# Optimization experiments

Measured on AMD Instinct MI355X. Metric: run time of the kernel, lower is better.

Reference implementation:

```python
import jax, jax.numpy as jnp
import numpy as np

D_MODEL = 1024
N_HEADS = 16
HEAD_DIM = D_MODEL // N_HEADS
ROPE_BASE = 10000.0


def setup_inputs() -> dict:
    key = jax.random.key(0)
    ks = jax.random.split(key, 9)
    s = 0.02
    inp = {
        "x": jax.random.normal(ks[0], (2, 2048, D_MODEL), dtype=jnp.float32),
        "Wq": jax.random.normal(ks[1], (D_MODEL, D_MODEL), dtype=jnp.float32) * s,
        "bq": jnp.zeros((D_MODEL,), dtype=jnp.float32),
        "Wk": jax.random.normal(ks[2], (D_MODEL, D_MODEL), dtype=jnp.float32) * s,
        "bk": jnp.zeros((D_MODEL,), dtype=jnp.float32),
        "Wv": jax.random.normal(ks[3], (D_MODEL, D_MODEL), dtype=jnp.float32) * s,
        "bv": jnp.zeros((D_MODEL,), dtype=jnp.float32),
        "Wo": jax.random.normal(ks[4], (D_MODEL, D_MODEL), dtype=jnp.float32) * s,
        "bo": jnp.zeros((D_MODEL,), dtype=jnp.float32),
    }
    return inp


def _rope_cos_sin(T, head_dim, dtype):
    inv_freq = 1.0 / (ROPE_BASE ** (jnp.arange(0, head_dim, 2, dtype=jnp.float32) / head_dim))
    pos = jnp.arange(T, dtype=jnp.float32)
    freqs = jnp.outer(pos, inv_freq)              # [T, head_dim/2]
    emb = jnp.concatenate([freqs, freqs], axis=-1)  # [T, head_dim]
    return jnp.cos(emb).astype(dtype), jnp.sin(emb).astype(dtype)


def _rotate_half(x):
    x1, x2 = jnp.split(x, 2, axis=-1)
    return jnp.concatenate([-x2, x1], axis=-1)


def reference(x, Wq, bq, Wk, bk, Wv, bv, Wo, bo):
    B, T, _ = x.shape
    H, Dh = N_HEADS, HEAD_DIM
    # projections (torch Linear: x @ W.T + b)
    q = (x @ Wq.T + bq).reshape(B, T, H, Dh).transpose(0, 2, 1, 3)  # [B,H,T,Dh]
    k = (x @ Wk.T + bk).reshape(B, T, H, Dh).transpose(0, 2, 1, 3)
    v = (x @ Wv.T + bv).reshape(B, T, H, Dh).transpose(0, 2, 1, 3)
    cos, sin = _rope_cos_sin(T, Dh, x.dtype)  # [T, Dh]
    cos = cos[None, None]
    sin = sin[None, None]
    q = q * cos + _rotate_half(q) * sin
    k = k * cos + _rotate_half(k) * sin
    scale = 1.0 / jnp.sqrt(jnp.asarray(Dh, dtype=x.dtype))
    attn = jnp.einsum("bhqd,bhkd->bhqk", q, k) * scale
    attn = jax.nn.softmax(attn, axis=-1)
    out = jnp.einsum("bhqk,bhkd->bhqd", attn, v)  # [B,H,T,Dh]
    out = out.transpose(0, 2, 1, 3).reshape(B, T, H * Dh)
    return out @ Wo.T + bo
```

## Files before the change

kernel.cpp:

```cpp
#include <hip/hip_runtime.h>
#include <hip/hip_bf16.h>
#include <cstdint>

#define D_MODEL 1024
#define NHEADS 16
#define HDIM 64
#define SEQ 2048
#define NBATCH 2
#define BT (NBATCH * SEQ)

typedef short bf16x8 __attribute__((ext_vector_type(8)));
typedef float f32x4 __attribute__((ext_vector_type(4)));
typedef unsigned short u16;
typedef unsigned int u32;

__device__ inline u16 f2bf(float f) {
    union { float f; u32 u; } x;
    x.f = f;
    u32 r = (x.u + 0x7fffu + ((x.u >> 16) & 1u)) >> 16;
    return (u16)r;
}

__device__ inline u32 pack2bf(float a, float b) {
    union { __hip_bfloat162 h; u32 u; } c;
    c.h = __float22bfloat162_rn(float2{a, b});
    return c.u;
}

__device__ inline float bf2f(u16 v) {
    union { u32 u; float f; } x;
    x.u = ((u32)v) << 16;
    return x.f;
}

__device__ inline void async_copy16(const u16* g, u16* l) {
    __builtin_amdgcn_global_load_lds((const __attribute__((address_space(1))) void*)g,
                                     (__attribute__((address_space(3))) void*)l, 16, 0, 0);
}

__device__ inline void permswap32(u32& a, u32& b) {
    asm("v_permlane32_swap_b32 %0, %1" : "+v"(a), "+v"(b));
}
__device__ inline void permswap16(u32& a, u32& b) {
    asm("v_permlane16_swap_b32 %0, %1" : "+v"(a), "+v"(b));
}

#define X4 (BT * D_MODEL / 4)
#define W4 (D_MODEL * D_MODEL / 4)
#define ROPE_N (SEQ * 32)

__global__ void prep_kernel(const float* __restrict__ x,
                            const float* __restrict__ wq, const float* __restrict__ wk,
                            const float* __restrict__ wv, const float* __restrict__ wo,
                            u16* __restrict__ xb,
                            u16* __restrict__ dq, u16* __restrict__ dk,
                            u16* __restrict__ dv, u16* __restrict__ dow,
                            float2* __restrict__ csT) {
    int idx = blockIdx.x * blockDim.x + threadIdx.x;
    if (idx < X4) {
        float4 v = ((const float4*)x)[idx];
        ushort4 o;
        o.x = f2bf(v.x); o.y = f2bf(v.y); o.z = f2bf(v.z); o.w = f2bf(v.w);
        ((ushort4*)xb)[idx] = o;
    } else if (idx < X4 + 4 * W4) {
        int j = idx - X4;
        int w = j >> 18, i = j & (W4 - 1);
        const float* s = (w == 0) ? wq : (w == 1) ? wk : (w == 2) ? wv : wo;
        u16* d = (w == 0) ? dq : (w == 1) ? dk : (w == 2) ? dv : dow;
        float4 v = ((const float4*)s)[i];
        ushort4 o;
        o.x = f2bf(v.x); o.y = f2bf(v.y); o.z = f2bf(v.z); o.w = f2bf(v.w);
        ((ushort4*)d)[i] = o;
    } else {
        int j = idx - (X4 + 4 * W4);
        if (j < ROPE_N) {
            int t = j >> 5, dm = j & 31;
            float invf = exp2f(-(float)dm * (13.287712379549449f / 32.0f));
            float ang = (float)t * invf;
            float s, c;
            sincosf(ang, &s, &c);
            csT[t * 32 + dm] = float2{c, s};
        }
    }
}

#define QSCALE 0.1803368801111204f
#define VPAD 132

__global__ __launch_bounds__(256) void gemm_qkv_kernel(
    const u16* __restrict__ xb,
    const u16* __restrict__ wqb, const u16* __restrict__ wkb, const u16* __restrict__ wvb,
    const float* __restrict__ bq, const float* __restrict__ bk, const float* __restrict__ bv,
    const float2* __restrict__ csT,
    u16* __restrict__ Qb, u16* __restrict__ Kb, u16* __restrict__ VTb) {
    __shared__ __align__(16) u16 smem[128 * VPAD];

    const int z = blockIdx.z;
    const u16* Bw = (z == 0) ? wqb : (z == 1) ? wkb : wvb;
    const float* bias = (z == 0) ? bq : (z == 1) ? bk : bv;

    const int tid = threadIdx.x;
    const int lane = tid & 63, wave = tid >> 6;
    const int waveM = wave >> 1, waveN = wave & 1;
    const int quad = lane >> 4, l16 = lane & 15;

    f32x4 acc[4][4];
#pragma unroll
    for (int mt = 0; mt < 4; ++mt)
#pragma unroll
        for (int nt = 0; nt < 4; ++nt)
            acc[mt][nt] = (f32x4){0.f, 0.f, 0.f, 0.f};

    const int srow = tid >> 2;
    const int scol = (tid & 3) << 3;
    const u16* Ag0 = xb + (size_t)(blockIdx.x * 128 + srow) * D_MODEL + scol;
    const u16* Ag1 = Ag0 + (size_t)64 * D_MODEL;
    const u16* Bg0 = Bw + (size_t)(blockIdx.y * 128 + srow) * D_MODEL + scol;
    const u16* Bg1 = Bg0 + (size_t)64 * D_MODEL;
    const int sidx = srow * 32 + scol;
    u16* As = smem;
    u16* Bs = smem + 8192;

    uint4 a0 = *(const uint4*)&Ag0[0];
    uint4 a1 = *(const uint4*)&Ag1[0];
    uint4 b0 = *(const uint4*)&Bg0[0];
    uint4 b1 = *(const uint4*)&Bg1[0];
    *(uint4*)&As[sidx] = a0;
    *(uint4*)&As[sidx + 2048] = a1;
    *(uint4*)&Bs[sidx] = b0;
    *(uint4*)&Bs[sidx + 2048] = b1;
    a0 = *(const uint4*)&Ag0[32];
    a1 = *(const uint4*)&Ag1[32];
    b0 = *(const uint4*)&Bg0[32];
    b1 = *(const uint4*)&Bg1[32];
    __syncthreads();

#pragma unroll 2
    for (int it = 0; it < 32; ++it) {
        const int cur = it & 1;
        if (it < 31) {
            u16* Ad = As + (cur ^ 1) * 4096;
            u16* Bd = Bs + (cur ^ 1) * 4096;
            *(uint4*)&Ad[sidx] = a0;
            *(uint4*)&Ad[sidx + 2048] = a1;
            *(uint4*)&Bd[sidx] = b0;
            *(uint4*)&Bd[sidx + 2048] = b1;
        }
        if (it < 30) {
            const int k = (it + 2) * 32;
            a0 = *(const uint4*)&Ag0[k];
            a1 = *(const uint4*)&Ag1[k];
            b0 = *(const uint4*)&Bg0[k];
            b1 = *(const uint4*)&Bg1[k];
        }
        const u16* Ac = As + cur * 4096;
        const u16* Bc = Bs + cur * 4096;
        bf16x8 af[4], bfr[4];
#pragma unroll
        for (int mt = 0; mt < 4; ++mt)
            af[mt] = *(const bf16x8*)&Ac[(waveM * 64 + mt * 16 + l16) * 32 + quad * 8];
#pragma unroll
        for (int nt = 0; nt < 4; ++nt)
            bfr[nt] = *(const bf16x8*)&Bc[(waveN * 64 + nt * 16 + l16) * 32 + quad * 8];
#pragma unroll
        for (int mt = 0; mt < 4; ++mt)
#pragma unroll
            for (int nt = 0; nt < 4; ++nt)
                acc[mt][nt] = __builtin_amdgcn_mfma_f32_16x16x32_bf16(af[mt], bfr[nt], acc[mt][nt], 0, 0, 0);
        __syncthreads();
    }

    const int gm0 = blockIdx.x * 128 + waveM * 64 + quad * 4;
    const int gn0 = blockIdx.y * 128 + waveN * 64 + l16;

    float bvv[4];
#pragma unroll
    for (int nt = 0; nt < 4; ++nt) bvv[nt] = bias[gn0 + nt * 16];
#pragma unroll
    for (int mt = 0; mt < 4; ++mt)
#pragma unroll
        for (int nt = 0; nt < 4; ++nt)
#pragma unroll
            for (int r = 0; r < 4; ++r) acc[mt][nt][r] += bvv[nt];

    if (z < 2) {
        u16* dst = (z == 0) ? Qb : Kb;
        const float post = (z == 0) ? QSCALE : 1.0f;
        const int h = 2 * blockIdx.y + waveN;
#pragma unroll
        for (int mt = 0; mt < 4; ++mt) {
#pragma unroll
            for (int r = 0; r < 4; ++r) {
                int gm = gm0 + mt * 16 + r;
                int t = gm & (SEQ - 1), b = gm >> 11;
                float2 cs0 = csT[t * 32 + l16];
                float2 cs1 = csT[t * 32 + 16 + l16];
                float a0f = acc[mt][0][r], a1f = acc[mt][1][r];
                float a2f = acc[mt][2][r], a3f = acc[mt][3][r];
                size_t base = ((size_t)(b * NHEADS + h) * SEQ + t) * HDIM;
                dst[base + l16]      = f2bf((a0f * cs0.x - a2f * cs0.y) * post);
                dst[base + l16 + 16] = f2bf((a1f * cs1.x - a3f * cs1.y) * post);
                dst[base + l16 + 32] = f2bf((a2f * cs0.x + a0f * cs0.y) * post);
                dst[base + l16 + 48] = f2bf((a3f * cs1.x + a1f * cs1.y) * post);
            }
        }
    } else {
        __syncthreads();
#pragma unroll
        for (int mt = 0; mt < 4; ++mt) {
            int t_local = waveM * 64 + mt * 16 + quad * 4;
#pragma unroll
            for (int nt = 0; nt < 4; ++nt) {
                int n_local = waveN * 64 + nt * 16 + l16;
                uint2 w;
                w.x = pack2bf(acc[mt][nt][0], acc[mt][nt][1]);
                w.y = pack2bf(acc[mt][nt][2], acc[mt][nt][3]);
                *(uint2*)&smem[n_local * VPAD + t_local] = w;
            }
        }
        __syncthreads();
        const int row = tid >> 1;
        const int hc = (tid & 1) * 64;
        const int n_g = blockIdx.y * 128 + row;
        const int h = n_g >> 6, d = n_g & 63;
        const int b = (blockIdx.x * 128) >> 11;
        const int t0 = ((blockIdx.x * 128) & (SEQ - 1)) + hc;
        u16* dst = &VTb[((size_t)(b * NHEADS + h) * HDIM + d) * SEQ + t0];
        const u16* src = &smem[row * VPAD + hc];
#pragma unroll
        for (int j = 0; j < 8; ++j)
            *(int4*)&dst[j * 8] = *(const int4*)&src[j * 8];
    }
}

#define LPAD 72

__global__ __launch_bounds__(256, 2) void flash_kernel(
    const u16* __restrict__ Qb, const u16* __restrict__ Kb, const u16* __restrict__ VTb,
    u16* __restrict__ Po0, u16* __restrict__ Po1, float* __restrict__ Ls) {
    __shared__ __align__(16) u16 Ks[2][64 * LPAD];
    __shared__ __align__(16) u16 VTs[2][64 * LPAD];

    const int tid = threadIdx.x;
    const int wave = tid >> 6, lane = tid & 63;
    const int quad = lane >> 4, l16 = lane & 15;
    const int bh = blockIdx.y;
    const int hf = blockIdx.z;
    const u16* Qh = Qb + (size_t)bh * SEQ * HDIM;
    const u16* Kh = Kb + ((size_t)bh * SEQ + hf * (SEQ / 2)) * HDIM;
    const u16* Vh = VTb + (size_t)bh * HDIM * SEQ + hf * (SEQ / 2);
    const int qblk = blockIdx.x * 256 + wave * 64;

    bf16x8 aq[4][2];
#pragma unroll
    for (int nt2 = 0; nt2 < 4; ++nt2)
#pragma unroll
        for (int ks = 0; ks < 2; ++ks)
            aq[nt2][ks] = *(const bf16x8*)&Qh[(qblk + nt2 * 16 + l16) * HDIM + ks * 32 + quad * 8];

    f32x4 o[4][4];
    float lsum[4] = {0.f, 0.f, 0.f, 0.f};
#pragma unroll
    for (int mt2 = 0; mt2 < 4; ++mt2)
#pragma unroll
        for (int nt = 0; nt < 4; ++nt) o[mt2][nt] = (f32x4){0.f, 0.f, 0.f, 0.f};

    const int lr = tid >> 2;
    const int lc = (tid & 3) * 16;
    const u16* Kg = Kh + (size_t)lr * HDIM + lc;
    const u16* Vg = Vh + (size_t)lr * SEQ + lc;
    const int sidx = lr * LPAD + lc;

    uint4 ka, kc, va, vc;
    ka = *(const uint4*)&Kg[0];
    kc = *(const uint4*)&Kg[8];
    va = *(const uint4*)&Vg[0];
    vc = *(const uint4*)&Vg[8];
    *(uint4*)&Ks[0][sidx] = ka;
    *(uint4*)&Ks[0][sidx + 8] = kc;
    *(uint4*)&VTs[0][sidx] = va;
    *(uint4*)&VTs[0][sidx + 8] = vc;
    ka = *(const uint4*)&Kg[(size_t)64 * HDIM];
    kc = *(const uint4*)&Kg[(size_t)64 * HDIM + 8];
    va = *(const uint4*)&Vg[64];
    vc = *(const uint4*)&Vg[64 + 8];
    __syncthreads();

#pragma unroll 2
    for (int it = 0; it < 16; ++it) {
        const int cur = it & 1;
        if (it < 15) {
            *(uint4*)&Ks[cur ^ 1][sidx] = ka;
            *(uint4*)&Ks[cur ^ 1][sidx + 8] = kc;
            *(uint4*)&VTs[cur ^ 1][sidx] = va;
            *(uint4*)&VTs[cur ^ 1][sidx + 8] = vc;
        }
        if (it < 14) {
            ka = *(const uint4*)&Kg[(size_t)(it + 2) * 64 * HDIM];
            kc = *(const uint4*)&Kg[(size_t)(it + 2) * 64 * HDIM + 8];
            va = *(const uint4*)&Vg[(it + 2) * 64];
            vc = *(const uint4*)&Vg[(it + 2) * 64 + 8];
        }
        const u16* Ksc = Ks[cur];
        const u16* Vsc = VTs[cur];

        f32x4 sacc[4][4];
#pragma unroll
        for (int mt = 0; mt < 4; ++mt)
#pragma unroll
            for (int nt2 = 0; nt2 < 4; ++nt2) sacc[mt][nt2] = (f32x4){0.f, 0.f, 0.f, 0.f};
#pragma unroll
        for (int ks = 0; ks < 2; ++ks) {
            bf16x8 kf[4];
#pragma unroll
            for (int mt = 0; mt < 4; ++mt)
                kf[mt] = *(const bf16x8*)&Ksc[(mt * 16 + l16) * LPAD + ks * 32 + quad * 8];
#pragma unroll
            for (int mt = 0; mt < 4; ++mt)
#pragma unroll
                for (int nt2 = 0; nt2 < 4; ++nt2)
                    sacc[mt][nt2] = __builtin_amdgcn_mfma_f32_16x16x32_bf16(kf[mt], aq[nt2][ks], sacc[mt][nt2], 0, 0, 0);
        }

        u32 pq[4][2][4];
#pragma unroll
        for (int nt2 = 0; nt2 < 4; ++nt2) {
            u32 w[4][2];
#pragma unroll
            for (int mt = 0; mt < 4; ++mt) {
                float p0 = __builtin_amdgcn_exp2f(sacc[mt][nt2][0]);
                float p1 = __builtin_amdgcn_exp2f(sacc[mt][nt2][1]);
                float p2 = __builtin_amdgcn_exp2f(sacc[mt][nt2][2]);
                float p3 = __builtin_amdgcn_exp2f(sacc[mt][nt2][3]);
                lsum[nt2] += (p0 + p1) + (p2 + p3);
                w[mt][0] = pack2bf(p0, p1);
                w[mt][1] = pack2bf(p2, p3);
            }
#pragma unroll
            for (int ks = 0; ks < 2; ++ks)
#pragma unroll
                for (int h = 0; h < 2; ++h) {
                    u32 a = w[2 * ks][h], b = w[2 * ks + 1][h];
                    permswap32(a, b);
                    permswap16(a, b);
                    pq[nt2][ks][h] = a;
                    pq[nt2][ks][2 + h] = b;
                }
        }

#pragma unroll
        for (int ks = 0; ks < 2; ++ks) {
            bf16x8 vf[4];
#pragma unroll
            for (int nt = 0; nt < 4; ++nt)
                vf[nt] = *(const bf16x8*)&Vsc[(nt * 16 + l16) * LPAD + ks * 32 + quad * 8];
#pragma unroll
            for (int mt2 = 0; mt2 < 4; ++mt2) {
                union { u32 u[4]; bf16x8 v; } pf;
                pf.u[0] = pq[mt2][ks][0];
                pf.u[1] = pq[mt2][ks][1];
                pf.u[2] = pq[mt2][ks][2];
                pf.u[3] = pq[mt2][ks][3];
#pragma unroll
                for (int nt = 0; nt < 4; ++nt)
                    o[mt2][nt] = __builtin_amdgcn_mfma_f32_16x16x32_bf16(pf.v, vf[nt], o[mt2][nt], 0, 0, 0);
            }
        }
        __syncthreads();
    }

#pragma unroll
    for (int nt2 = 0; nt2 < 4; ++nt2) {
        lsum[nt2] += __shfl_xor(lsum[nt2], 16, 64);
        lsum[nt2] += __shfl_xor(lsum[nt2], 32, 64);
    }

    const int b = bh >> 4, h = bh & 15;
    u16* dst = hf ? Po1 : Po0;
#pragma unroll
    for (int mt2 = 0; mt2 < 4; ++mt2) {
#pragma unroll
        for (int nt = 0; nt < 4; ++nt) {
            int d = nt * 16 + l16;
#pragma unroll
            for (int r = 0; r < 4; ++r) {
                int q = qblk + mt2 * 16 + quad * 4 + r;
                dst[((size_t)(b * SEQ + q)) * D_MODEL + h * HDIM + d] = f2bf(o[mt2][nt][r]);
            }
        }
    }
    if (quad == 0) {
#pragma unroll
        for (int nt2 = 0; nt2 < 4; ++nt2) {
            int q = qblk + nt2 * 16 + l16;
            Ls[hf * (32 * SEQ) + bh * SEQ + q] = lsum[nt2];
        }
    }
}

__global__ __launch_bounds__(256) void gemm_out_kernel(
    const u16* __restrict__ Po0, const u16* __restrict__ Po1, const float* __restrict__ Ls,
    const u16* __restrict__ wob, const float* __restrict__ bo, float* __restrict__ dout) {
    __shared__ __align__(16) u16 Asmem[64 * 32];
    __shared__ __align__(16) u16 Bsmem[128 * 32];

    const int tid = threadIdx.x;
    const int lane = tid & 63, wave = tid >> 6;
    const int waveM = wave >> 1, waveN = wave & 1;
    const int quad = lane >> 4, l16 = lane & 15;

    f32x4 acc[2][4];
#pragma unroll
    for (int mt = 0; mt < 2; ++mt)
#pragma unroll
        for (int nt = 0; nt < 4; ++nt) acc[mt][nt] = (f32x4){0.f, 0.f, 0.f, 0.f};

    const int srow = tid >> 2;
    const int scol = (tid & 3) << 3;
    const int q = blockIdx.x * 64 + srow;
    const int b = q >> 11, t = q & (SEQ - 1);
    const size_t arow = (size_t)q * D_MODEL + scol;
    const u16* Bg0 = wob + (size_t)(blockIdx.y * 128 + srow) * D_MODEL + scol;
    const u16* Bg1 = Bg0 + (size_t)64 * D_MODEL;
    u16* Al = Asmem + srow * 32 + scol;
    u16* Bl0 = Bsmem + srow * 32 + scol;
    u16* Bl1 = Bl0 + 64 * 32;

    float rinvh[NHEADS];
    {
        const int bhq0 = b * NHEADS * SEQ + t;
#pragma unroll
        for (int h = 0; h < NHEADS; ++h) {
            int bhq = bhq0 + h * SEQ;
            rinvh[h] = 1.0f / (Ls[bhq] + Ls[32 * SEQ + bhq]);
        }
    }

    uint4 A0 = *(const uint4*)&Po0[arow];
    uint4 A1 = *(const uint4*)&Po1[arow];

    for (int k0 = 0; k0 < D_MODEL; k0 += 32) {
        __syncthreads();
        float rinv = rinvh[(k0 + scol) >> 6];
        const u16* p0 = (const u16*)&A0;
        const u16* p1 = (const u16*)&A1;
        uint4 wv;
        u32* wvp = (u32*)&wv;
#pragma unroll
        for (int j = 0; j < 4; ++j) {
            float s0 = (bf2f(p0[2 * j]) + bf2f(p1[2 * j])) * rinv;
            float s1 = (bf2f(p0[2 * j + 1]) + bf2f(p1[2 * j + 1])) * rinv;
            wvp[j] = pack2bf(s0, s1);
        }
        *(uint4*)Al = wv;
        async_copy16(Bg0 + k0, Bl0);
        async_copy16(Bg1 + k0, Bl1);
        if (k0 + 32 < D_MODEL) {
            A0 = *(const uint4*)&Po0[arow + k0 + 32];
            A1 = *(const uint4*)&Po1[arow + k0 + 32];
        }
        __syncthreads();
        bf16x8 af[2], bfr[4];
#pragma unroll
        for (int mt = 0; mt < 2; ++mt)
            af[mt] = *(const bf16x8*)&Asmem[(waveM * 32 + mt * 16 + l16) * 32 + quad * 8];
#pragma unroll
        for (int nt = 0; nt < 4; ++nt)
            bfr[nt] = *(const bf16x8*)&Bsmem[(waveN * 64 + nt * 16 + l16) * 32 + quad * 8];
#pragma unroll
        for (int mt = 0; mt < 2; ++mt)
#pragma unroll
            for (int nt = 0; nt < 4; ++nt)
                acc[mt][nt] = __builtin_amdgcn_mfma_f32_16x16x32_bf16(af[mt], bfr[nt], acc[mt][nt], 0, 0, 0);
    }

    const int gm0 = blockIdx.x * 64 + waveM * 32 + quad * 4;
    const int gn0 = blockIdx.y * 128 + waveN * 64 + l16;

    float bvv[4];
#pragma unroll
    for (int nt = 0; nt < 4; ++nt) bvv[nt] = bo[gn0 + nt * 16];
#pragma unroll
    for (int mt = 0; mt < 2; ++mt)
#pragma unroll
        for (int nt = 0; nt < 4; ++nt)
#pragma unroll
            for (int r = 0; r < 4; ++r)
                dout[(size_t)(gm0 + mt * 16 + r) * D_MODEL + gn0 + nt * 16] = acc[mt][nt][r] + bvv[nt];
}

extern "C" void kernel_launch(void* const* d_in, const int* in_sizes, int n_in,
                              void* d_out, int out_size, void* d_ws, size_t ws_size,
                              hipStream_t stream) {
    const float* x  = (const float*)d_in[0];
    const float* Wq = (const float*)d_in[1];
    const float* bq = (const float*)d_in[2];
    const float* Wk = (const float*)d_in[3];
    const float* bk = (const float*)d_in[4];
    const float* Wv = (const float*)d_in[5];
    const float* bv = (const float*)d_in[6];
    const float* Wo = (const float*)d_in[7];
    const float* bo = (const float*)d_in[8];
    float* dout = (float*)d_out;

    char* ws = (char*)d_ws;
    size_t off = 0;
    u16* xb  = (u16*)(ws + off); off += (size_t)BT * D_MODEL * 2;
    u16* wqb = (u16*)(ws + off); off += (size_t)D_MODEL * D_MODEL * 2;
    u16* wkb = (u16*)(ws + off); off += (size_t)D_MODEL * D_MODEL * 2;
    u16* wvb = (u16*)(ws + off); off += (size_t)D_MODEL * D_MODEL * 2;
    u16* wob = (u16*)(ws + off); off += (size_t)D_MODEL * D_MODEL * 2;
    u16* Qb  = (u16*)(ws + off); off += (size_t)BT * D_MODEL * 2;
    u16* Kb  = (u16*)(ws + off); off += (size_t)BT * D_MODEL * 2;
    u16* VTb = (u16*)(ws + off); off += (size_t)BT * D_MODEL * 2;
    u16* Po0 = (u16*)(ws + off); off += (size_t)BT * D_MODEL * 2;
    float2* csT = (float2*)(ws + off); off += (size_t)SEQ * 32 * 8;
    float* Ls   = (float*)(ws + off); off += (size_t)2 * 32 * SEQ * 4;
    u16* Po1 = xb;

    const int prepN = X4 + 4 * W4 + ROPE_N;
    prep_kernel<<<dim3((prepN + 255) / 256), 256, 0, stream>>>(
        x, Wq, Wk, Wv, Wo, xb, wqb, wkb, wvb, wob, csT);
    gemm_qkv_kernel<<<dim3(BT / 128, D_MODEL / 128, 3), 256, 0, stream>>>(
        xb, wqb, wkb, wvb, bq, bk, bv, csT, Qb, Kb, VTb);
    flash_kernel<<<dim3(SEQ / 256, NBATCH * NHEADS, 2), 256, 0, stream>>>(
        Qb, Kb, VTb, Po0, Po1, Ls);
    gemm_out_kernel<<<dim3(BT / 64, D_MODEL / 128), 256, 0, stream>>>(
        Po0, Po1, Ls, wob, bo, dout);
}
```

Baseline: 204.2 us.

## Fuse x fp32-to-bf16 conversion into QKV GEMM, async-load weights, prioritize MFMA

Drops the separate conversion of x to bf16 in the prep kernel. The QKV GEMM now reads fp32 x directly and packs it to bf16 as it stages tiles into LDS, which removes a 16 MB intermediate write and read. Weight tiles are loaded with global_load_lds async copies instead of passing through registers. The flash kernel raises wave priority around its MFMA blocks. The trade-off is that the QKV GEMM reads x in fp32 three times (once per z slice), doubling A-operand traffic, and the async copies rely on the existing barrier for ordering.

```diff
diff --git a/kernel.cpp b/kernel.cpp
--- a/kernel.cpp
+++ b/kernel.cpp
@@ -27,6 +27,15 @@
     return c.u;
 }
 
+__device__ inline uint4 pack8bf(const float4& a, const float4& b) {
+    uint4 r;
+    r.x = pack2bf(a.x, a.y);
+    r.y = pack2bf(a.z, a.w);
+    r.z = pack2bf(b.x, b.y);
+    r.w = pack2bf(b.z, b.w);
+    return r;
+}
+
 __device__ inline float bf2f(u16 v) {
     union { u32 u; float f; } x;
     x.u = ((u32)v) << 16;
@@ -45,26 +54,17 @@
     asm("v_permlane16_swap_b32 %0, %1" : "+v"(a), "+v"(b));
 }
 
-#define X4 (BT * D_MODEL / 4)
 #define W4 (D_MODEL * D_MODEL / 4)
 #define ROPE_N (SEQ * 32)
 
-__global__ void prep_kernel(const float* __restrict__ x,
-                            const float* __restrict__ wq, const float* __restrict__ wk,
+__global__ void prep_kernel(const float* __restrict__ wq, const float* __restrict__ wk,
                             const float* __restrict__ wv, const float* __restrict__ wo,
-                            u16* __restrict__ xb,
                             u16* __restrict__ dq, u16* __restrict__ dk,
                             u16* __restrict__ dv, u16* __restrict__ dow,
                             float2* __restrict__ csT) {
     int idx = blockIdx.x * blockDim.x + threadIdx.x;
-    if (idx < X4) {
-        float4 v = ((const float4*)x)[idx];
-        ushort4 o;
-        o.x = f2bf(v.x); o.y = f2bf(v.y); o.z = f2bf(v.z); o.w = f2bf(v.w);
-        ((ushort4*)xb)[idx] = o;
-    } else if (idx < X4 + 4 * W4) {
-        int j = idx - X4;
-        int w = j >> 18, i = j & (W4 - 1);
+    if (idx < 4 * W4) {
+        int w = idx >> 18, i = idx & (W4 - 1);
         const float* s = (w == 0) ? wq : (w == 1) ? wk : (w == 2) ? wv : wo;
         u16* d = (w == 0) ? dq : (w == 1) ? dk : (w == 2) ? dv : dow;
         float4 v = ((const float4*)s)[i];
@@ -72,7 +72,7 @@
         o.x = f2bf(v.x); o.y = f2bf(v.y); o.z = f2bf(v.z); o.w = f2bf(v.w);
         ((ushort4*)d)[i] = o;
     } else {
-        int j = idx - (X4 + 4 * W4);
+        int j = idx - 4 * W4;
         if (j < ROPE_N) {
             int t = j >> 5, dm = j & 31;
             float invf = exp2f(-(float)dm * (13.287712379549449f / 32.0f));
@@ -88,7 +88,7 @@
 #define VPAD 132
 
 __global__ __launch_bounds__(256) void gemm_qkv_kernel(
-    const u16* __restrict__ xb,
+    const float* __restrict__ x,
     const u16* __restrict__ wqb, const u16* __restrict__ wkb, const u16* __restrict__ wvb,
     const float* __restrict__ bq, const float* __restrict__ bk, const float* __restrict__ bv,
     const float2* __restrict__ csT,
@@ -113,26 +113,26 @@
 
     const int srow = tid >> 2;
     const int scol = (tid & 3) << 3;
-    const u16* Ag0 = xb + (size_t)(blockIdx.x * 128 + srow) * D_MODEL + scol;
-    const u16* Ag1 = Ag0 + (size_t)64 * D_MODEL;
+    const float* Ag0 = x + (size_t)(blockIdx.x * 128 + srow) * D_MODEL + scol;
+    const float* Ag1 = Ag0 + (size_t)64 * D_MODEL;
     const u16* Bg0 = Bw + (size_t)(blockIdx.y * 128 + srow) * D_MODEL + scol;
     const u16* Bg1 = Bg0 + (size_t)64 * D_MODEL;
     const int sidx = srow * 32 + scol;
     u16* As = smem;
     u16* Bs = smem + 8192;
 
-    uint4 a0 = *(const uint4*)&Ag0[0];
-    uint4 a1 = *(const uint4*)&Ag1[0];
-    uint4 b0 = *(const uint4*)&Bg0[0];
-    uint4 b1 = *(const uint4*)&Bg1[0];
-    *(uint4*)&As[sidx] = a0;
-    *(uint4*)&As[sidx + 2048] = a1;
-    *(uint4*)&Bs[sidx] = b0;
-    *(uint4*)&Bs[sidx + 2048] = b1;
-    a0 = *(const uint4*)&Ag0[32];
-    a1 = *(const uint4*)&Ag1[32];
-    b0 = *(const uint4*)&Bg0[32];
-    b1 = *(const uint4*)&Bg1[32];
+    float4 af0 = *(const float4*)&Ag0[0];
+    float4 af1 = *(const float4*)&Ag0[4];
+    float4 af2 = *(const float4*)&Ag1[0];
+    float4 af3 = *(const float4*)&Ag1[4];
+    *(uint4*)&As[sidx] = pack8bf(af0, af1);
+    *(uint4*)&As[sidx + 2048] = pack8bf(af2, af3);
+    async_copy16(Bg0, Bs + sidx);
+    async_copy16(Bg1, Bs + sidx + 2048);
+    af0 = *(const float4*)&Ag0[32];
+    af1 = *(const float4*)&Ag0[36];
+    af2 = *(const float4*)&Ag1[32];
+    af3 = *(const float4*)&Ag1[36];
     __syncthreads();
 
 #pragma unroll 2
@@ -140,18 +140,18 @@
         const int cur = it & 1;
         if (it < 31) {
             u16* Ad = As + (cur ^ 1) * 4096;
+            *(uint4*)&Ad[sidx] = pack8bf(af0, af1);
+            *(uint4*)&Ad[sidx + 2048] = pack8bf(af2, af3);
             u16* Bd = Bs + (cur ^ 1) * 4096;
-            *(uint4*)&Ad[sidx] = a0;
-            *(uint4*)&Ad[sidx + 2048] = a1;
-            *(uint4*)&Bd[sidx] = b0;
-            *(uint4*)&Bd[sidx + 2048] = b1;
+            async_copy16(Bg0 + (it + 1) * 32, Bd + sidx);
+            async_copy16(Bg1 + (it + 1) * 32, Bd + sidx + 2048);
         }
         if (it < 30) {
             const int k = (it + 2) * 32;
-            a0 = *(const uint4*)&Ag0[k];
-            a1 = *(const uint4*)&Ag1[k];
-            b0 = *(const uint4*)&Bg0[k];
-            b1 = *(const uint4*)&Bg1[k];
+            af0 = *(const float4*)&Ag0[k];
+            af1 = *(const float4*)&Ag0[k + 4];
+            af2 = *(const float4*)&Ag1[k];
+            af3 = *(const float4*)&Ag1[k + 4];
         }
         const u16* Ac = As + cur * 4096;
         const u16* Bc = Bs + cur * 4096;
@@ -315,11 +315,13 @@
 #pragma unroll
             for (int mt = 0; mt < 4; ++mt)
                 kf[mt] = *(const bf16x8*)&Ksc[(mt * 16 + l16) * LPAD + ks * 32 + quad * 8];
+            __builtin_amdgcn_s_setprio(1);
 #pragma unroll
             for (int mt = 0; mt < 4; ++mt)
 #pragma unroll
                 for (int nt2 = 0; nt2 < 4; ++nt2)
                     sacc[mt][nt2] = __builtin_amdgcn_mfma_f32_16x16x32_bf16(kf[mt], aq[nt2][ks], sacc[mt][nt2], 0, 0, 0);
+            __builtin_amdgcn_s_setprio(0);
         }
 
         u32 pq[4][2][4];
@@ -354,6 +356,7 @@
 #pragma unroll
             for (int nt = 0; nt < 4; ++nt)
                 vf[nt] = *(const bf16x8*)&Vsc[(nt * 16 + l16) * LPAD + ks * 32 + quad * 8];
+            __builtin_amdgcn_s_setprio(1);
 #pragma unroll
             for (int mt2 = 0; mt2 < 4; ++mt2) {
                 union { u32 u[4]; bf16x8 v; } pf;
@@ -365,6 +368,7 @@
                 for (int nt = 0; nt < 4; ++nt)
                     o[mt2][nt] = __builtin_amdgcn_mfma_f32_16x16x32_bf16(pf.v, vf[nt], o[mt2][nt], 0, 0, 0);
             }
+            __builtin_amdgcn_s_setprio(0);
         }
         __syncthreads();
     }
@@ -505,7 +509,7 @@
 
     char* ws = (char*)d_ws;
     size_t off = 0;
-    u16* xb  = (u16*)(ws + off); off += (size_t)BT * D_MODEL * 2;
+    u16* Po1 = (u16*)(ws + off); off += (size_t)BT * D_MODEL * 2;
     u16* wqb = (u16*)(ws + off); off += (size_t)D_MODEL * D_MODEL * 2;
     u16* wkb = (u16*)(ws + off); off += (size_t)D_MODEL * D_MODEL * 2;
     u16* wvb = (u16*)(ws + off); off += (size_t)D_MODEL * D_MODEL * 2;
@@ -516,13 +520,12 @@
     u16* Po0 = (u16*)(ws + off); off += (size_t)BT * D_MODEL * 2;
     float2* csT = (float2*)(ws + off); off += (size_t)SEQ * 32 * 8;
     float* Ls   = (float*)(ws + off); off += (size_t)2 * 32 * SEQ * 4;
-    u16* Po1 = xb;
-
-    const int prepN = X4 + 4 * W4 + ROPE_N;
+
+    const int prepN = 4 * W4 + ROPE_N;
     prep_kernel<<<dim3((prepN + 255) / 256), 256, 0, stream>>>(
-        x, Wq, Wk, Wv, Wo, xb, wqb, wkb, wvb, wob, csT);
+        Wq, Wk, Wv, Wo, wqb, wkb, wvb, wob, csT);
     gemm_qkv_kernel<<<dim3(BT / 128, D_MODEL / 128, 3), 256, 0, stream>>>(
-        xb, wqb, wkb, wvb, bq, bk, bv, csT, Qb, Kb, VTb);
+        x, wqb, wkb, wvb, bq, bk, bv, csT, Qb, Kb, VTb);
     flash_kernel<<<dim3(SEQ / 256, NBATCH * NHEADS, 2), 256, 0, stream>>>(
         Qb, Kb, VTb, Po0, Po1, Ls);
     gemm_out_kernel<<<dim3(BT / 64, D_MODEL / 128), 256, 0, stream>>>(
```

After: 231.4 us. +13.3%, slower.
